# Performance work log

Measured on AMD Instinct MI355X. Metric: run time of the kernel, lower is better.

Reference implementation:

```python
import jax, jax.numpy as jnp
import numpy as np

B, T, D, A = 64, 2048, 512, 128

def setup_inputs() -> dict:
    key = jax.random.key(0)
    k_x, k_w1, k_b1, k_w2, k_b2 = jax.random.split(key, 5)
    s1 = 1.0 / np.sqrt(D)
    s2 = 1.0 / np.sqrt(A)
    return {
        "x": jax.random.normal(k_x, (B, T, D), dtype=jnp.float32),
        "W1": jax.random.uniform(k_w1, (D, A), minval=-s1, maxval=s1, dtype=jnp.float32),
        "b1": jax.random.uniform(k_b1, (A,), minval=-s1, maxval=s1, dtype=jnp.float32),
        "W2": jax.random.uniform(k_w2, (A, 1), minval=-s2, maxval=s2, dtype=jnp.float32),
        "b2": jax.random.uniform(k_b2, (1,), minval=-s2, maxval=s2, dtype=jnp.float32),
    }

def reference(x, W1, b1, W2, b2):
    # attention scores: [B, T, 1]
    h = jnp.tanh(jnp.einsum('btd,da->bta', x, W1) + b1)
    scores = jnp.einsum('bta,ao->bto', h, W2) + b2
    w = jax.nn.softmax(scores, axis=1)              # [B, T, 1]
    mu = jnp.sum(x * w, axis=1)                     # [B, D]
    var = jnp.sum((x - mu[:, None, :]) ** 2 * w, axis=1)
    std = jnp.sqrt(var + 1e-6)
    return jnp.concatenate([mu, std], axis=-1)      # [B, 2D]
```

## Files before the change

kernel.cpp:

```cpp
#include <hip/hip_runtime.h>
#include <hip/hip_bf16.h>
#include <math.h>

#define B_ 64
#define T_ 2048
#define D_ 512
#define A_ 128
#define CHUNK 64
#define NCHUNK (T_ / CHUNK)

typedef __bf16 bf16x8 __attribute__((ext_vector_type(8)));
typedef float  f32x4  __attribute__((ext_vector_type(4)));

__global__ __launch_bounds__(256) void prep_kernel(
    const float* __restrict__ W1, __hip_bfloat16* __restrict__ W1T)
{
    int idx = blockIdx.x * 256 + threadIdx.x;
    int k = idx >> 7;
    int n = idx & 127;
    W1T[n * D_ + k] = __float2bfloat16(W1[idx]);
}

__device__ inline bf16x8 cvt8(float4 a, float4 b) {
    bf16x8 r;
    r[0] = (__bf16)a.x; r[1] = (__bf16)a.y; r[2] = (__bf16)a.z; r[3] = (__bf16)a.w;
    r[4] = (__bf16)b.x; r[5] = (__bf16)b.y; r[6] = (__bf16)b.z; r[7] = (__bf16)b.w;
    return r;
}

__device__ inline float fast_tanh(float v) {
    v = fminf(fmaxf(v, -15.f), 15.f);
    float e = __expf(2.f * v);
    return (e - 1.f) / (e + 1.f);
}

__global__ __launch_bounds__(256) void fused_kernel(
    const float* __restrict__ x, const __hip_bfloat16* __restrict__ W1T_,
    const float* __restrict__ b1, const float* __restrict__ W2,
    const float* __restrict__ b2,
    float* __restrict__ pmu, float* __restrict__ pm2, float* __restrict__ pz)
{
    const __bf16* W1T = (const __bf16*)W1T_;
    const int tid  = threadIdx.x;
    const int wave = tid >> 6;
    const int lane = tid & 63;
    const int col  = lane & 15;
    const int kgrp = lane >> 4;

    const int  blk = blockIdx.x;
    const long tokbase = (long)blk * CHUNK + wave * 16;

    f32x4 acc[8];
#pragma unroll
    for (int mt = 0; mt < 8; mt++) acc[mt] = (f32x4){0.f, 0.f, 0.f, 0.f};

    const float* xp = x + (tokbase + col) * D_;
    const __bf16* wp = W1T + (long)col * D_;

#pragma unroll 4
    for (int ks = 0; ks < 16; ks++) {
        const int klane = ks * 32 + kgrp * 8;
        float4 a0 = *(const float4*)(xp + klane);
        float4 a1 = *(const float4*)(xp + klane + 4);
        bf16x8 bf = cvt8(a0, a1);
#pragma unroll
        for (int mt = 0; mt < 8; mt++) {
            bf16x8 af = *(const bf16x8*)(wp + (long)mt * 16 * D_ + klane);
            acc[mt] = __builtin_amdgcn_mfma_f32_16x16x32_bf16(af, bf, acc[mt], 0, 0, 0);
        }
    }

    float p = 0.f;
#pragma unroll
    for (int mt = 0; mt < 8; mt++) {
#pragma unroll
        for (int r = 0; r < 4; r++) {
            int n = mt * 16 + kgrp * 4 + r;
            p += fast_tanh(acc[mt][r] + b1[n]) * W2[n];
        }
    }
    p += __shfl_xor(p, 16, 64);
    p += __shfl_xor(p, 32, 64);

    __shared__ float se[CHUNK];
    if (lane < 16)
        se[wave * 16 + col] = __expf(p + b2[0]);
    __syncthreads();

    const int tg = tid >> 7;
    const int dq = tid & 127;
    const float* xb = x + (long)blk * CHUNK * D_ + dq * 4;

    float4 mu = {0.f, 0.f, 0.f, 0.f};
    float4 m2 = {0.f, 0.f, 0.f, 0.f};
#pragma unroll 4
    for (int t = tg; t < CHUNK; t += 2) {
        float e = se[t];
        float4 xv = *(const float4*)(xb + (long)t * D_);
        mu.x = fmaf(e, xv.x, mu.x);
        mu.y = fmaf(e, xv.y, mu.y);
        mu.z = fmaf(e, xv.z, mu.z);
        mu.w = fmaf(e, xv.w, mu.w);
        m2.x = fmaf(e * xv.x, xv.x, m2.x);
        m2.y = fmaf(e * xv.y, xv.y, m2.y);
        m2.z = fmaf(e * xv.z, xv.z, m2.z);
        m2.w = fmaf(e * xv.w, xv.w, m2.w);
    }

    __shared__ float4 smu[256];
    __shared__ float4 sm2[256];
    smu[tid] = mu;
    sm2[tid] = m2;
    __syncthreads();

    if (tid < 128) {
        float4 a = smu[tid], c = smu[tid + 128];
        float4 e = sm2[tid], f = sm2[tid + 128];
        a.x += c.x; a.y += c.y; a.z += c.z; a.w += c.w;
        e.x += f.x; e.y += f.y; e.z += f.z; e.w += f.w;
        *(float4*)(pmu + (long)blk * D_ + dq * 4) = a;
        *(float4*)(pm2 + (long)blk * D_ + dq * 4) = e;
    }
    if (tid == 0) {
        float z = 0.f;
#pragma unroll
        for (int t = 0; t < CHUNK; t++) z += se[t];
        pz[blk] = z;
    }
}

__global__ __launch_bounds__(256) void finalize_kernel(
    const float* __restrict__ pmu, const float* __restrict__ pm2,
    const float* __restrict__ pz, float* __restrict__ out)
{
    const int b = blockIdx.x;
    const int tid = threadIdx.x;

    __shared__ float zsh;
    float z = (tid < NCHUNK) ? pz[b * NCHUNK + tid] : 0.f;
#pragma unroll
    for (int off = 1; off < 32; off <<= 1) z += __shfl_xor(z, off, 64);
    if (tid == 0) zsh = z;
    __syncthreads();
    const float invz = 1.0f / zsh;

#pragma unroll
    for (int i = 0; i < 2; i++) {
        int d = tid + i * 256;
        float mu = 0.f, m2 = 0.f;
#pragma unroll
        for (int c = 0; c < NCHUNK; c++) {
            mu += pmu[((long)b * NCHUNK + c) * D_ + d];
            m2 += pm2[((long)b * NCHUNK + c) * D_ + d];
        }
        mu *= invz;
        m2 *= invz;
        out[(long)b * (2 * D_) + d] = mu;
        out[(long)b * (2 * D_) + D_ + d] = sqrtf(fmaxf(m2 - mu * mu, 0.f) + 1e-6f);
    }
}

extern "C" void kernel_launch(void* const* d_in, const int* in_sizes, int n_in,
                              void* d_out, int out_size, void* d_ws, size_t ws_size,
                              hipStream_t stream) {
    const float* x  = (const float*)d_in[0];
    const float* W1 = (const float*)d_in[1];
    const float* b1 = (const float*)d_in[2];
    const float* W2 = (const float*)d_in[3];
    const float* b2 = (const float*)d_in[4];
    float* out = (float*)d_out;

    const int nblk = (B_ * T_) / CHUNK;
    float* ws = (float*)d_ws;
    float* pmu = ws;
    float* pm2 = pmu + (long)nblk * D_;
    float* pz  = pm2 + (long)nblk * D_;
    __hip_bfloat16* W1T = (__hip_bfloat16*)(pz + nblk);

    prep_kernel<<<256, 256, 0, stream>>>(W1, W1T);
    fused_kernel<<<nblk, 256, 0, stream>>>(x, W1T, b1, W2, b2, pmu, pm2, pz);
    finalize_kernel<<<B_, 256, 0, stream>>>(pmu, pm2, pz, out);
}
```

Measured before the change: 473.9 us.

## Stage x tile in LDS via direct global-to-LDS loads, reuse for stats

Each block now handles 16 tokens with one wave. The x tile is staged into LDS with global_load_lds using an XOR-swizzled layout, and that staged copy feeds both the MFMA projection and the weighted mean/second-moment accumulation, so x is read from global memory once rather than twice. The finalize kernel is split across 8 blocks per batch to handle the now 4x larger partial arrays. The partial buffers grow fourfold, which adds write and finalize traffic, and single-wave blocks with 32KB of LDS may limit occupancy.

Measured after the change: 489.5 us. 3.3% more time.

```diff
diff --git a/kernel.cpp b/kernel.cpp
--- a/kernel.cpp
+++ b/kernel.cpp
@@ -6,8 +6,8 @@
 #define T_ 2048
 #define D_ 512
 #define A_ 128
-#define CHUNK 64
-#define NCHUNK (T_ / CHUNK)
+#define TPB 128
+#define NTILE (B_ * TPB)
 
 typedef __bf16 bf16x8 __attribute__((ext_vector_type(8)));
 typedef float  f32x4  __attribute__((ext_vector_type(4)));
@@ -21,10 +21,10 @@
     W1T[n * D_ + k] = __float2bfloat16(W1[idx]);
 }
 
-__device__ inline bf16x8 cvt8(float4 a, float4 b) {
+__device__ inline bf16x8 cvt8(f32x4 a, f32x4 b) {
     bf16x8 r;
-    r[0] = (__bf16)a.x; r[1] = (__bf16)a.y; r[2] = (__bf16)a.z; r[3] = (__bf16)a.w;
-    r[4] = (__bf16)b.x; r[5] = (__bf16)b.y; r[6] = (__bf16)b.z; r[7] = (__bf16)b.w;
+    r[0] = (__bf16)a[0]; r[1] = (__bf16)a[1]; r[2] = (__bf16)a[2]; r[3] = (__bf16)a[3];
+    r[4] = (__bf16)b[0]; r[5] = (__bf16)b[1]; r[6] = (__bf16)b[2]; r[7] = (__bf16)b[3];
     return r;
 }
 
@@ -34,38 +34,48 @@
     return (e - 1.f) / (e + 1.f);
 }
 
-__global__ __launch_bounds__(256) void fused_kernel(
+__global__ __launch_bounds__(64) void fused_kernel(
     const float* __restrict__ x, const __hip_bfloat16* __restrict__ W1T_,
     const float* __restrict__ b1, const float* __restrict__ W2,
     const float* __restrict__ b2,
     float* __restrict__ pmu, float* __restrict__ pm2, float* __restrict__ pz)
 {
+    __shared__ float xs[16 * 512];
     const __bf16* W1T = (const __bf16*)W1T_;
-    const int tid  = threadIdx.x;
-    const int wave = tid >> 6;
-    const int lane = tid & 63;
+    const int lane = threadIdx.x;
     const int col  = lane & 15;
     const int kgrp = lane >> 4;
 
-    const int  blk = blockIdx.x;
-    const long tokbase = (long)blk * CHUNK + wave * 16;
+    const int  tile    = blockIdx.x;
+    const long tokbase = (long)tile * 16;
+
+    for (int ks = 0; ks < 16; ks++) {
+        const float* gp = x + (tokbase + (long)(col ^ ks)) * D_ + ks * 32 + kgrp * 8;
+        float* lp = xs + ks * 512;
+        __builtin_amdgcn_global_load_lds(
+            (__attribute__((address_space(1))) const void*)gp,
+            (__attribute__((address_space(3))) void*)lp, 16, 0, 0);
+        __builtin_amdgcn_global_load_lds(
+            (__attribute__((address_space(1))) const void*)(gp + 4),
+            (__attribute__((address_space(3))) void*)(lp + 256), 16, 0, 0);
+    }
+    __syncthreads();
 
     f32x4 acc[8];
 #pragma unroll
     for (int mt = 0; mt < 8; mt++) acc[mt] = (f32x4){0.f, 0.f, 0.f, 0.f};
 
-    const float* xp = x + (tokbase + col) * D_;
     const __bf16* wp = W1T + (long)col * D_;
 
 #pragma unroll 4
     for (int ks = 0; ks < 16; ks++) {
-        const int klane = ks * 32 + kgrp * 8;
-        float4 a0 = *(const float4*)(xp + klane);
-        float4 a1 = *(const float4*)(xp + klane + 4);
+        const int uoff = ks * 512 + (kgrp * 16 + (col ^ ks)) * 4;
+        f32x4 a0 = *(const f32x4*)&xs[uoff];
+        f32x4 a1 = *(const f32x4*)&xs[uoff + 256];
         bf16x8 bf = cvt8(a0, a1);
 #pragma unroll
         for (int mt = 0; mt < 8; mt++) {
-            bf16x8 af = *(const bf16x8*)(wp + (long)mt * 16 * D_ + klane);
+            bf16x8 af = *(const bf16x8*)(wp + (long)mt * 16 * D_ + ks * 32 + kgrp * 8);
             acc[mt] = __builtin_amdgcn_mfma_f32_16x16x32_bf16(af, bf, acc[mt], 0, 0, 0);
         }
     }
@@ -82,81 +92,76 @@
     p += __shfl_xor(p, 16, 64);
     p += __shfl_xor(p, 32, 64);
 
-    __shared__ float se[CHUNK];
-    if (lane < 16)
-        se[wave * 16 + col] = __expf(p + b2[0]);
-    __syncthreads();
+    const float e = __expf(p + b2[0]);
 
-    const int tg = tid >> 7;
-    const int dq = tid & 127;
-    const float* xb = x + (long)blk * CHUNK * D_ + dq * 4;
+    const int ksl = col;
+    const int g   = kgrp;
+    f32x4 mu0 = {0.f,0.f,0.f,0.f}, mu1 = {0.f,0.f,0.f,0.f};
+    f32x4 m20 = {0.f,0.f,0.f,0.f}, m21 = {0.f,0.f,0.f,0.f};
 
-    float4 mu = {0.f, 0.f, 0.f, 0.f};
-    float4 m2 = {0.f, 0.f, 0.f, 0.f};
 #pragma unroll 4
-    for (int t = tg; t < CHUNK; t += 2) {
-        float e = se[t];
-        float4 xv = *(const float4*)(xb + (long)t * D_);
-        mu.x = fmaf(e, xv.x, mu.x);
-        mu.y = fmaf(e, xv.y, mu.y);
-        mu.z = fmaf(e, xv.z, mu.z);
-        mu.w = fmaf(e, xv.w, mu.w);
-        m2.x = fmaf(e * xv.x, xv.x, m2.x);
-        m2.y = fmaf(e * xv.y, xv.y, m2.y);
-        m2.z = fmaf(e * xv.z, xv.z, m2.z);
-        m2.w = fmaf(e * xv.w, xv.w, m2.w);
+    for (int t = 0; t < 16; t++) {
+        float et = __shfl(e, t, 64);
+        const int ubase = ksl * 512 + (g * 16 + (t ^ ksl)) * 4;
+        f32x4 v0 = *(const f32x4*)&xs[ubase];
+        f32x4 v1 = *(const f32x4*)&xs[ubase + 256];
+        f32x4 w0 = et * v0;
+        f32x4 w1 = et * v1;
+        mu0 += w0;  mu1 += w1;
+        m20 += w0 * v0;  m21 += w1 * v1;
     }
 
-    __shared__ float4 smu[256];
-    __shared__ float4 sm2[256];
-    smu[tid] = mu;
-    sm2[tid] = m2;
-    __syncthreads();
+    const long obase = (long)tile * D_ + ksl * 32 + g * 8;
+    *(f32x4*)&pmu[obase]     = mu0;
+    *(f32x4*)&pmu[obase + 4] = mu1;
+    *(f32x4*)&pm2[obase]     = m20;
+    *(f32x4*)&pm2[obase + 4] = m21;
 
-    if (tid < 128) {
-        float4 a = smu[tid], c = smu[tid + 128];
-        float4 e = sm2[tid], f = sm2[tid + 128];
-        a.x += c.x; a.y += c.y; a.z += c.z; a.w += c.w;
-        e.x += f.x; e.y += f.y; e.z += f.z; e.w += f.w;
-        *(float4*)(pmu + (long)blk * D_ + dq * 4) = a;
-        *(float4*)(pm2 + (long)blk * D_ + dq * 4) = e;
-    }
-    if (tid == 0) {
-        float z = 0.f;
-#pragma unroll
-        for (int t = 0; t < CHUNK; t++) z += se[t];
-        pz[blk] = z;
-    }
+    float z = e;
+    z += __shfl_xor(z, 1, 64);
+    z += __shfl_xor(z, 2, 64);
+    z += __shfl_xor(z, 4, 64);
+    z += __shfl_xor(z, 8, 64);
+    if (lane == 0) pz[tile] = z;
 }
 
 __global__ __launch_bounds__(256) void finalize_kernel(
     const float* __restrict__ pmu, const float* __restrict__ pm2,
     const float* __restrict__ pz, float* __restrict__ out)
 {
-    const int b = blockIdx.x;
+    const int bid = blockIdx.x;
+    const int b   = bid >> 3;
+    const int dc  = (bid & 7) << 6;
     const int tid = threadIdx.x;
+    const int tg  = tid >> 6;
+    const int dl  = tid & 63;
+    const int d   = dc + dl;
 
-    __shared__ float zsh;
-    float z = (tid < NCHUNK) ? pz[b * NCHUNK + tid] : 0.f;
+    __shared__ float zsh[2];
+    float z = (tid < TPB) ? pz[b * TPB + tid] : 0.f;
 #pragma unroll
-    for (int off = 1; off < 32; off <<= 1) z += __shfl_xor(z, off, 64);
-    if (tid == 0) zsh = z;
+    for (int off = 1; off < 64; off <<= 1) z += __shfl_xor(z, off, 64);
+    if (tid < TPB && (tid & 63) == 0) zsh[tid >> 6] = z;
+
+    float mu = 0.f, m2 = 0.f;
+    for (int c = tg; c < TPB; c += 4) {
+        mu += pmu[((long)b * TPB + c) * D_ + d];
+        m2 += pm2[((long)b * TPB + c) * D_ + d];
+    }
+    __shared__ float smu[4][64];
+    __shared__ float sm2[4][64];
+    smu[tg][dl] = mu;
+    sm2[tg][dl] = m2;
     __syncthreads();
-    const float invz = 1.0f / zsh;
 
-#pragma unroll
-    for (int i = 0; i < 2; i++) {
-        int d = tid + i * 256;
-        float mu = 0.f, m2 = 0.f;
-#pragma unroll
-        for (int c = 0; c < NCHUNK; c++) {
-            mu += pmu[((long)b * NCHUNK + c) * D_ + d];
-            m2 += pm2[((long)b * NCHUNK + c) * D_ + d];
-        }
-        mu *= invz;
-        m2 *= invz;
-        out[(long)b * (2 * D_) + d] = mu;
-        out[(long)b * (2 * D_) + D_ + d] = sqrtf(fmaxf(m2 - mu * mu, 0.f) + 1e-6f);
+    if (tid < 64) {
+        const float invz = 1.0f / (zsh[0] + zsh[1]);
+        float M = (smu[0][tid] + smu[1][tid]) + (smu[2][tid] + smu[3][tid]);
+        float S = (sm2[0][tid] + sm2[1][tid]) + (sm2[2][tid] + sm2[3][tid]);
+        M *= invz;
+        S *= invz;
+        out[(long)b * (2 * D_) + dc + tid] = M;
+        out[(long)b * (2 * D_) + D_ + dc + tid] = sqrtf(fmaxf(S - M * M, 0.f) + 1e-6f);
     }
 }
 
@@ -170,14 +175,13 @@
     const float* b2 = (const float*)d_in[4];
     float* out = (float*)d_out;
 
-    const int nblk = (B_ * T_) / CHUNK;
     float* ws = (float*)d_ws;
     float* pmu = ws;
-    float* pm2 = pmu + (long)nblk * D_;
-    float* pz  = pm2 + (long)nblk * D_;
-    __hip_bfloat16* W1T = (__hip_bfloat16*)(pz + nblk);
+    float* pm2 = pmu + (long)NTILE * D_;
+    float* pz  = pm2 + (long)NTILE * D_;
+    __hip_bfloat16* W1T = (__hip_bfloat16*)(pz + NTILE);
 
     prep_kernel<<<256, 256, 0, stream>>>(W1, W1T);
-    fused_kernel<<<nblk, 256, 0, stream>>>(x, W1T, b1, W2, b2, pmu, pm2, pz);
-    finalize_kernel<<<B_, 256, 0, stream>>>(pmu, pm2, pz, out);
+    fused_kernel<<<NTILE, 64, 0, stream>>>(x, W1T, b1, W2, b2, pmu, pm2, pz);
+    finalize_kernel<<<B_ * 8, 256, 0, stream>>>(pmu, pm2, pz, out);
 }
```

## Split fused kernel into MFMA scores kernel with 4x token tiling and pooling kernel

Applied to the files above, without the earlier changes.

The fused score-plus-pooling kernel is split in two. A scores kernel now has each wave handle 64 tokens, reusing each W1 fragment load across four MFMA token tiles and writing exp(score) to workspace. A separate pooling kernel then re-reads x in 128-token chunks to build the partial weighted moments and partition sums. This cuts redundant W1 loads and gives better MFMA reuse, but x is now streamed twice (about 268MB each pass) instead of reusing it from cache inside one block.

New measurement: 488.4 us. 1.03x slower.

```diff
diff --git a/kernel.cpp b/kernel.cpp
--- a/kernel.cpp
+++ b/kernel.cpp
@@ -6,8 +6,8 @@
 #define T_ 2048
 #define D_ 512
 #define A_ 128
-#define CHUNK 64
-#define NCHUNK (T_ / CHUNK)
+#define CH 128
+#define NCH (T_ / CH)
 
 typedef __bf16 bf16x8 __attribute__((ext_vector_type(8)));
 typedef float  f32x4  __attribute__((ext_vector_type(4)));
@@ -34,11 +34,10 @@
     return (e - 1.f) / (e + 1.f);
 }
 
-__global__ __launch_bounds__(256) void fused_kernel(
+__global__ __launch_bounds__(256) void scores_kernel(
     const float* __restrict__ x, const __hip_bfloat16* __restrict__ W1T_,
     const float* __restrict__ b1, const float* __restrict__ W2,
-    const float* __restrict__ b2,
-    float* __restrict__ pmu, float* __restrict__ pm2, float* __restrict__ pz)
+    const float* __restrict__ b2, float* __restrict__ ew)
 {
     const __bf16* W1T = (const __bf16*)W1T_;
     const int tid  = threadIdx.x;
@@ -47,64 +46,92 @@
     const int col  = lane & 15;
     const int kgrp = lane >> 4;
 
-    const int  blk = blockIdx.x;
-    const long tokbase = (long)blk * CHUNK + wave * 16;
-
-    f32x4 acc[8];
-#pragma unroll
-    for (int mt = 0; mt < 8; mt++) acc[mt] = (f32x4){0.f, 0.f, 0.f, 0.f};
-
-    const float* xp = x + (tokbase + col) * D_;
+    const long tokbase = (long)blockIdx.x * 256 + wave * 64;
+
+    f32x4 acc[8][4];
+#pragma unroll
+    for (int mt = 0; mt < 8; mt++)
+#pragma unroll
+        for (int tt = 0; tt < 4; tt++)
+            acc[mt][tt] = (f32x4){0.f, 0.f, 0.f, 0.f};
+
+    const float*  xp = x + (tokbase + col) * D_;
     const __bf16* wp = W1T + (long)col * D_;
 
-#pragma unroll 4
+#pragma unroll 2
     for (int ks = 0; ks < 16; ks++) {
         const int klane = ks * 32 + kgrp * 8;
-        float4 a0 = *(const float4*)(xp + klane);
-        float4 a1 = *(const float4*)(xp + klane + 4);
-        bf16x8 bf = cvt8(a0, a1);
+        bf16x8 bf[4];
+#pragma unroll
+        for (int tt = 0; tt < 4; tt++) {
+            float4 a0 = *(const float4*)(xp + (long)tt * 16 * D_ + klane);
+            float4 a1 = *(const float4*)(xp + (long)tt * 16 * D_ + klane + 4);
+            bf[tt] = cvt8(a0, a1);
+        }
 #pragma unroll
         for (int mt = 0; mt < 8; mt++) {
             bf16x8 af = *(const bf16x8*)(wp + (long)mt * 16 * D_ + klane);
-            acc[mt] = __builtin_amdgcn_mfma_f32_16x16x32_bf16(af, bf, acc[mt], 0, 0, 0);
-        }
-    }
-
-    float p = 0.f;
+#pragma unroll
+            for (int tt = 0; tt < 4; tt++)
+                acc[mt][tt] = __builtin_amdgcn_mfma_f32_16x16x32_bf16(af, bf[tt], acc[mt][tt], 0, 0, 0);
+        }
+    }
+
+    float p[4] = {0.f, 0.f, 0.f, 0.f};
 #pragma unroll
     for (int mt = 0; mt < 8; mt++) {
 #pragma unroll
         for (int r = 0; r < 4; r++) {
             int n = mt * 16 + kgrp * 4 + r;
-            p += fast_tanh(acc[mt][r] + b1[n]) * W2[n];
-        }
-    }
-    p += __shfl_xor(p, 16, 64);
-    p += __shfl_xor(p, 32, 64);
-
-    __shared__ float se[CHUNK];
-    if (lane < 16)
-        se[wave * 16 + col] = __expf(p + b2[0]);
-    __syncthreads();
-
-    const int tg = tid >> 7;
+            float bb = b1[n];
+            float ww = W2[n];
+#pragma unroll
+            for (int tt = 0; tt < 4; tt++)
+                p[tt] += fast_tanh(acc[mt][tt][r] + bb) * ww;
+        }
+    }
+#pragma unroll
+    for (int tt = 0; tt < 4; tt++) {
+        p[tt] += __shfl_xor(p[tt], 16, 64);
+        p[tt] += __shfl_xor(p[tt], 32, 64);
+    }
+    if (lane < 16) {
+        float bias = b2[0];
+#pragma unroll
+        for (int tt = 0; tt < 4; tt++)
+            ew[tokbase + tt * 16 + col] = __expf(p[tt] + bias);
+    }
+}
+
+__global__ __launch_bounds__(256) void pool_partial_kernel(
+    const float* __restrict__ x, const float* __restrict__ ew,
+    float* __restrict__ pmu, float* __restrict__ pm2, float* __restrict__ pz)
+{
+    const int blk = blockIdx.x;
+    const int b = blk >> 4;
+    const int t0 = (blk & 15) * CH;
+    const int tid = threadIdx.x;
+    const int half = tid >> 7;
     const int dq = tid & 127;
-    const float* xb = x + (long)blk * CHUNK * D_ + dq * 4;
+
+    const float* wb = ew + (long)b * T_ + t0;
+    const float* xb = x + ((long)b * T_ + t0) * D_ + dq * 4;
 
     float4 mu = {0.f, 0.f, 0.f, 0.f};
     float4 m2 = {0.f, 0.f, 0.f, 0.f};
+
 #pragma unroll 4
-    for (int t = tg; t < CHUNK; t += 2) {
-        float e = se[t];
+    for (int t = half; t < CH; t += 2) {
+        float wt = wb[t];
         float4 xv = *(const float4*)(xb + (long)t * D_);
-        mu.x = fmaf(e, xv.x, mu.x);
-        mu.y = fmaf(e, xv.y, mu.y);
-        mu.z = fmaf(e, xv.z, mu.z);
-        mu.w = fmaf(e, xv.w, mu.w);
-        m2.x = fmaf(e * xv.x, xv.x, m2.x);
-        m2.y = fmaf(e * xv.y, xv.y, m2.y);
-        m2.z = fmaf(e * xv.z, xv.z, m2.z);
-        m2.w = fmaf(e * xv.w, xv.w, m2.w);
+        mu.x = fmaf(wt, xv.x, mu.x);
+        mu.y = fmaf(wt, xv.y, mu.y);
+        mu.z = fmaf(wt, xv.z, mu.z);
+        mu.w = fmaf(wt, xv.w, mu.w);
+        m2.x = fmaf(wt * xv.x, xv.x, m2.x);
+        m2.y = fmaf(wt * xv.y, xv.y, m2.y);
+        m2.z = fmaf(wt * xv.z, xv.z, m2.z);
+        m2.w = fmaf(wt * xv.w, xv.w, m2.w);
     }
 
     __shared__ float4 smu[256];
@@ -120,12 +147,12 @@
         e.x += f.x; e.y += f.y; e.z += f.z; e.w += f.w;
         *(float4*)(pmu + (long)blk * D_ + dq * 4) = a;
         *(float4*)(pm2 + (long)blk * D_ + dq * 4) = e;
-    }
-    if (tid == 0) {
-        float z = 0.f;
-#pragma unroll
-        for (int t = 0; t < CHUNK; t++) z += se[t];
-        pz[blk] = z;
+    } else if (tid >= 192) {
+        int l = tid - 192;
+        float z = wb[l] + wb[l + 64];
+#pragma unroll
+        for (int off = 1; off < 64; off <<= 1) z += __shfl_xor(z, off, 64);
+        if (l == 0) pz[blk] = z;
     }
 }
 
@@ -137,10 +164,12 @@
     const int tid = threadIdx.x;
 
     __shared__ float zsh;
-    float z = (tid < NCHUNK) ? pz[b * NCHUNK + tid] : 0.f;
-#pragma unroll
-    for (int off = 1; off < 32; off <<= 1) z += __shfl_xor(z, off, 64);
-    if (tid == 0) zsh = z;
+    if (tid < 64) {
+        float z = (tid < NCH) ? pz[b * NCH + tid] : 0.f;
+#pragma unroll
+        for (int off = 1; off < 16; off <<= 1) z += __shfl_xor(z, off, 64);
+        if (tid == 0) zsh = z;
+    }
     __syncthreads();
     const float invz = 1.0f / zsh;
 
@@ -149,9 +178,9 @@
         int d = tid + i * 256;
         float mu = 0.f, m2 = 0.f;
 #pragma unroll
-        for (int c = 0; c < NCHUNK; c++) {
-            mu += pmu[((long)b * NCHUNK + c) * D_ + d];
-            m2 += pm2[((long)b * NCHUNK + c) * D_ + d];
+        for (int c = 0; c < NCH; c++) {
+            mu += pmu[((long)b * NCH + c) * D_ + d];
+            m2 += pm2[((long)b * NCH + c) * D_ + d];
         }
         mu *= invz;
         m2 *= invz;
@@ -170,14 +199,16 @@
     const float* b2 = (const float*)d_in[4];
     float* out = (float*)d_out;
 
-    const int nblk = (B_ * T_) / CHUNK;
-    float* ws = (float*)d_ws;
-    float* pmu = ws;
+    const int nblk = B_ * NCH;
+    float* ws  = (float*)d_ws;
+    float* ew  = ws;
+    float* pmu = ew + (long)B_ * T_;
     float* pm2 = pmu + (long)nblk * D_;
     float* pz  = pm2 + (long)nblk * D_;
     __hip_bfloat16* W1T = (__hip_bfloat16*)(pz + nblk);
 
     prep_kernel<<<256, 256, 0, stream>>>(W1, W1T);
-    fused_kernel<<<nblk, 256, 0, stream>>>(x, W1T, b1, W2, b2, pmu, pm2, pz);
+    scores_kernel<<<(B_ * T_) / 256, 256, 0, stream>>>(x, W1T, b1, W2, b2, ew);
+    pool_partial_kernel<<<nblk, 256, 0, stream>>>(x, ew, pmu, pm2, pz);
     finalize_kernel<<<B_, 256, 0, stream>>>(pmu, pm2, pz, out);
 }
```
